# Performance work log

Hardware: AMD Instinct MI355X
Metric: run time of the kernel (lower is better)

The kernel has to match this reference:

```python
import jax, jax.numpy as jnp
import numpy as np

N_EMBED = 40
HEAD_SIZE = 10
N_HEADS = 4
LN_EPS = 1e-5


def _layernorm(x, g, b):
    mu = jnp.mean(x, axis=-1, keepdims=True)
    var = jnp.mean(jnp.square(x - mu), axis=-1, keepdims=True)
    return (x - mu) * jax.lax.rsqrt(var + LN_EPS) * g + b


def setup_inputs() -> dict:
    key = jax.random.key(0)
    ks = jax.random.split(key, 12)
    B, T = 16, 2048
    s = 1.0 / np.sqrt(N_EMBED)
    return {
        "x": jax.random.normal(ks[0], (B, T, N_EMBED), dtype=jnp.float32),
        # per-head Q/K/V weights stacked: [H, n_embed, head_size]
        "Wq": jax.random.normal(ks[1], (N_HEADS, N_EMBED, HEAD_SIZE), dtype=jnp.float32) * s,
        "Wk": jax.random.normal(ks[2], (N_HEADS, N_EMBED, HEAD_SIZE), dtype=jnp.float32) * s,
        "Wv": jax.random.normal(ks[3], (N_HEADS, N_EMBED, HEAD_SIZE), dtype=jnp.float32) * s,
        "Wp": jax.random.normal(ks[4], (N_EMBED, N_EMBED), dtype=jnp.float32) * s,
        "bp": jnp.zeros((N_EMBED,), dtype=jnp.float32),
        "W1": jax.random.normal(ks[5], (N_EMBED, N_EMBED), dtype=jnp.float32) * s,
        "b1": jnp.zeros((N_EMBED,), dtype=jnp.float32),
        "W2": jax.random.normal(ks[6], (N_EMBED, N_EMBED), dtype=jnp.float32) * s,
        "b2": jnp.zeros((N_EMBED,), dtype=jnp.float32),
        "g1": jnp.ones((N_EMBED,), dtype=jnp.float32),
        "be1": jnp.zeros((N_EMBED,), dtype=jnp.float32),
        "g2": jnp.ones((N_EMBED,), dtype=jnp.float32),
        "be2": jnp.zeros((N_EMBED,), dtype=jnp.float32),
    }


def reference(x, Wq, Wk, Wv, Wp, bp, W1, b1, W2, b2, g1, be1, g2, be2):
    B, T, D = x.shape
    # --- pre-norm (note: original overwrites x, so residual uses ln1(x)) ---
    x = _layernorm(x, g1, be1)
    # --- multi-head attention (faithful to source: scores = k @ q^T, no scale, no mask) ---
    q = jnp.einsum("btd,hde->bhte", x, Wq)  # [B,H,T,hs]
    k = jnp.einsum("btd,hde->bhte", x, Wk)
    v = jnp.einsum("btd,hde->bhte", x, Wv)
    w = jnp.einsum("bhie,bhje->bhij", k, q)  # k @ q.transpose(-2,-1)
    w = jax.nn.softmax(w, axis=-1)
    out = jnp.einsum("bhij,bhje->bhie", w, v)  # [B,H,T,hs]
    out = jnp.transpose(out, (0, 2, 1, 3)).reshape(B, T, D)  # concat heads
    out = out @ Wp + bp
    x = x + out
    # --- second norm + FFN (residual uses ln2(x), as in source) ---
    x = _layernorm(x, g2, be2)
    h = jax.nn.relu(x @ W1 + b1)
    x = x + (h @ W2 + b2)
    return x
```

## Files before the change

### kernel.cpp

```cpp
#include <hip/hip_runtime.h>
#include <math.h>

namespace {

using bf16x8 = __attribute__((ext_vector_type(8))) short;
using f32x4  = __attribute__((ext_vector_type(4))) float;

constexpr int D   = 40;
constexpr int HS  = 10;
constexpr int NH  = 4;
constexpr int TT  = 2048;
constexpr int BB  = 16;
constexpr int ROWS = BB * TT;
constexpr int PE  = 16;
constexpr int VR  = 11;
constexpr float LOG2E = 1.4426950408889634f;

__device__ inline unsigned short f2b(float x) {
    unsigned int u = __float_as_uint(x);
    unsigned int r = (u + 0x7fffu + ((u >> 16) & 1u)) >> 16;
    return (unsigned short)r;
}

__device__ inline f32x4 mfma32(bf16x8 a, bf16x8 b, f32x4 c) {
    return __builtin_amdgcn_mfma_f32_16x16x32_bf16(a, b, c, 0, 0, 0);
}

__device__ inline float dot40(const float* __restrict__ xr,
                              const float* __restrict__ w) {
    float s0 = 0.f, s1 = 0.f, s2 = 0.f, s3 = 0.f;
    const float4* w4 = reinterpret_cast<const float4*>(w);
    #pragma unroll
    for (int i = 0; i < 10; ++i) {
        float4 t = w4[i];
        s0 = fmaf(xr[4*i+0], t.x, s0);
        s1 = fmaf(xr[4*i+1], t.y, s1);
        s2 = fmaf(xr[4*i+2], t.z, s2);
        s3 = fmaf(xr[4*i+3], t.w, s3);
    }
    return (s0 + s1) + (s2 + s3);
}

__global__ __launch_bounds__(256) void k_ln_qkv(
    const float* __restrict__ x,  const float* __restrict__ Wq,
    const float* __restrict__ Wk, const float* __restrict__ Wv,
    const float* __restrict__ g1, const float* __restrict__ be1,
    float* __restrict__ xn, unsigned short* __restrict__ qb,
    unsigned short* __restrict__ kb, unsigned short* __restrict__ vT)
{
    __shared__ float wt_s[3*NH*HS*D];
    __shared__ float g_s[D], b_s[D];
    const int tid = threadIdx.x;
    for (int i = tid; i < NH*D*HS; i += 256) {
        const int h = i / (D*HS), r = i % (D*HS);
        const int d = r / HS, e = r % HS;
        const int to = (h*HS + e)*D + d;
        wt_s[to]              = Wq[i];
        wt_s[NH*HS*D + to]    = Wk[i];
        wt_s[2*NH*HS*D + to]  = Wv[i];
    }
    if (tid < D) { g_s[tid] = g1[tid]; b_s[tid] = be1[tid]; }
    __syncthreads();

    const int gid = blockIdx.x * 256 + tid;
    const int row = gid >> 2;
    const int h   = gid & 3;

    float xr[D];
    const float4* xp = reinterpret_cast<const float4*>(x + (size_t)row * D);
    #pragma unroll
    for (int i = 0; i < D/4; ++i) {
        float4 t4 = xp[i];
        xr[4*i+0]=t4.x; xr[4*i+1]=t4.y; xr[4*i+2]=t4.z; xr[4*i+3]=t4.w;
    }
    float mu = 0.f;
    #pragma unroll
    for (int d = 0; d < D; ++d) mu += xr[d];
    mu *= (1.f/D);
    float var = 0.f;
    #pragma unroll
    for (int d = 0; d < D; ++d) { float dd = xr[d]-mu; var += dd*dd; }
    var *= (1.f/D);
    const float rs = rsqrtf(var + 1e-5f);
    #pragma unroll
    for (int d = 0; d < D; ++d) xr[d] = (xr[d]-mu)*rs*g_s[d] + b_s[d];

    if (h == 0) {
        float4* xo = reinterpret_cast<float4*>(xn + (size_t)row * D);
        #pragma unroll
        for (int i = 0; i < D/4; ++i) {
            float4 t4; t4.x=xr[4*i+0]; t4.y=xr[4*i+1]; t4.z=xr[4*i+2]; t4.w=xr[4*i+3];
            xo[i] = t4;
        }
    }

    const int b = row >> 11;
    const int t = row & (TT-1);
    const int bh = b*NH + h;

    float aq[HS], ak[HS], av[HS];
    #pragma unroll
    for (int e = 0; e < HS; ++e) {
        aq[e] = dot40(xr, &wt_s[(h*HS + e)*D]);
        ak[e] = dot40(xr, &wt_s[NH*HS*D + (h*HS + e)*D]);
        av[e] = dot40(xr, &wt_s[2*NH*HS*D + (h*HS + e)*D]);
    }

    union { unsigned short u[PE]; uint4 v4[2]; } Uq, Uk;
    #pragma unroll
    for (int e = 0; e < PE; ++e) {
        Uq.u[e] = (e < HS) ? f2b(aq[e] * LOG2E) : (unsigned short)0;
        Uk.u[e] = (e < HS) ? f2b(ak[e]) : (unsigned short)0;
    }
    uint4* qp4 = reinterpret_cast<uint4*>(qb + ((size_t)bh*TT + t)*PE);
    uint4* kp4 = reinterpret_cast<uint4*>(kb + ((size_t)bh*TT + t)*PE);
    qp4[0] = Uq.v4[0]; qp4[1] = Uq.v4[1];
    kp4[0] = Uk.v4[0]; kp4[1] = Uk.v4[1];
    #pragma unroll
    for (int e = 0; e < HS; ++e)
        vT[((size_t)bh*VR + e)*TT + t] = f2b(av[e]);
    vT[((size_t)bh*VR + HS)*TT + t] = 0x3F80;
}

__global__ __launch_bounds__(256, 4) void k_attn(
    const unsigned short* __restrict__ qb, const unsigned short* __restrict__ kb,
    const unsigned short* __restrict__ vT, float* __restrict__ ao)
{
    __shared__ __align__(16) unsigned short PT[4][2][16][40];
    const int w    = threadIdx.x >> 6;
    const int lane = threadIdx.x & 63;
    const int g    = lane >> 4;
    const int li   = lane & 15;
    const int bh   = blockIdx.y;
    const int i0   = blockIdx.x * 64 + w * 16;
    const size_t bT = (size_t)bh * TT;

    const bf16x8 zero8 = {0,0,0,0,0,0,0,0};
    const f32x4  zacc  = {0.f,0.f,0.f,0.f};

    bf16x8 kf = zero8;
    if (g < 2) kf = *reinterpret_cast<const bf16x8*>(kb + (bT + i0 + li)*PE + 8*g);

    f32x4 accA = zacc, accB = zacc;
    const unsigned short* vrow = vT + ((size_t)bh*VR + (li <= HS ? li : 0))*TT;
    const unsigned short* qrow = qb + (bT + li)*PE + 8*g;

    for (int it = 0; it < TT/64; ++it) {
        const int jA = it * 32;
        const int jB = jA + TT/2;

        bf16x8 a0A=zero8, a1A=zero8, a0B=zero8, a1B=zero8;
        if (g < 2) {
            a0A = *reinterpret_cast<const bf16x8*>(qrow + (size_t)(jA     )*PE);
            a1A = *reinterpret_cast<const bf16x8*>(qrow + (size_t)(jA + 16)*PE);
            a0B = *reinterpret_cast<const bf16x8*>(qrow + (size_t)(jB     )*PE);
            a1B = *reinterpret_cast<const bf16x8*>(qrow + (size_t)(jB + 16)*PE);
        }
        bf16x8 vfA=zero8, vfB=zero8;
        if (li <= HS) {
            vfA = *reinterpret_cast<const bf16x8*>(vrow + jA + 8*g);
            vfB = *reinterpret_cast<const bf16x8*>(vrow + jB + 8*g);
        }

        f32x4 sA0 = mfma32(a0A, kf, zacc);
        f32x4 sA1 = mfma32(a1A, kf, zacc);
        f32x4 sB0 = mfma32(a0B, kf, zacc);
        f32x4 sB1 = mfma32(a1B, kf, zacc);

        const float pA0 = __builtin_amdgcn_exp2f(sA0[0]), pA1 = __builtin_amdgcn_exp2f(sA0[1]);
        const float pA2 = __builtin_amdgcn_exp2f(sA0[2]), pA3 = __builtin_amdgcn_exp2f(sA0[3]);
        const float pA4 = __builtin_amdgcn_exp2f(sA1[0]), pA5 = __builtin_amdgcn_exp2f(sA1[1]);
        const float pA6 = __builtin_amdgcn_exp2f(sA1[2]), pA7 = __builtin_amdgcn_exp2f(sA1[3]);
        const float pB0 = __builtin_amdgcn_exp2f(sB0[0]), pB1 = __builtin_amdgcn_exp2f(sB0[1]);
        const float pB2 = __builtin_amdgcn_exp2f(sB0[2]), pB3 = __builtin_amdgcn_exp2f(sB0[3]);
        const float pB4 = __builtin_amdgcn_exp2f(sB1[0]), pB5 = __builtin_amdgcn_exp2f(sB1[1]);
        const float pB6 = __builtin_amdgcn_exp2f(sB1[2]), pB7 = __builtin_amdgcn_exp2f(sB1[3]);

        unsigned int wA0,wA1,wA2,wA3, wB0,wB1,wB2,wB3;
        asm("v_cvt_pk_bf16_f32 %0, %1, %2" : "=v"(wA0) : "v"(pA0), "v"(pA1));
        asm("v_cvt_pk_bf16_f32 %0, %1, %2" : "=v"(wA1) : "v"(pA2), "v"(pA3));
        asm("v_cvt_pk_bf16_f32 %0, %1, %2" : "=v"(wA2) : "v"(pA4), "v"(pA5));
        asm("v_cvt_pk_bf16_f32 %0, %1, %2" : "=v"(wA3) : "v"(pA6), "v"(pA7));
        asm("v_cvt_pk_bf16_f32 %0, %1, %2" : "=v"(wB0) : "v"(pB0), "v"(pB1));
        asm("v_cvt_pk_bf16_f32 %0, %1, %2" : "=v"(wB1) : "v"(pB2), "v"(pB3));
        asm("v_cvt_pk_bf16_f32 %0, %1, %2" : "=v"(wB2) : "v"(pB4), "v"(pB5));
        asm("v_cvt_pk_bf16_f32 %0, %1, %2" : "=v"(wB3) : "v"(pB6), "v"(pB7));

        *reinterpret_cast<uint2*>(&PT[w][0][li][4*g])      = make_uint2(wA0, wA1);
        *reinterpret_cast<uint2*>(&PT[w][0][li][16 + 4*g]) = make_uint2(wA2, wA3);
        *reinterpret_cast<uint2*>(&PT[w][1][li][4*g])      = make_uint2(wB0, wB1);
        *reinterpret_cast<uint2*>(&PT[w][1][li][16 + 4*g]) = make_uint2(wB2, wB3);

        bf16x8 pfA = *reinterpret_cast<const bf16x8*>(&PT[w][0][li][8*g]);
        bf16x8 pfB = *reinterpret_cast<const bf16x8*>(&PT[w][1][li][8*g]);

        accA = mfma32(vfA, pfA, accA);
        accB = mfma32(vfB, pfB, accB);
    }

    const f32x4 acc = accA + accB;
    const float l = __shfl(acc[2], 32 + li);
    const float linv = 1.f / l;
    float* orow = ao + (bT + i0 + li) * HS;
    #pragma unroll
    for (int r = 0; r < 4; ++r) {
        const int e = 4*g + r;
        if (e < HS) orow[e] = acc[r] * linv;
    }
}

__global__ __launch_bounds__(256) void k_epilogue(
    const float* __restrict__ attn, const float* __restrict__ xn,
    const float* __restrict__ Wp, const float* __restrict__ bp,
    const float* __restrict__ W1, const float* __restrict__ b1,
    const float* __restrict__ W2, const float* __restrict__ b2,
    const float* __restrict__ g2, const float* __restrict__ be2,
    float* __restrict__ out)
{
    __shared__ float wp_s[D*D], w1_s[D*D], w2_s[D*D];
    __shared__ float bp_s[D], b1_s[D], b2_s[D], g_s[D], be_s[D];
    const int tid = threadIdx.x;
    for (int i = tid; i < D*D; i += 256) { wp_s[i]=Wp[i]; w1_s[i]=W1[i]; w2_s[i]=W2[i]; }
    if (tid < D) {
        bp_s[tid]=bp[tid]; b1_s[tid]=b1[tid]; b2_s[tid]=b2[tid];
        g_s[tid]=g2[tid]; be_s[tid]=be2[tid];
    }
    __syncthreads();

    const int gid  = blockIdx.x * 256 + tid;
    const int row  = gid >> 1;
    const int half = gid & 1;
    const int b0   = half * 20;
    const int b    = row >> 11;
    const int t    = row & (TT-1);

    float cat[D];
    #pragma unroll
    for (int h = 0; h < NH; ++h) {
        const float2* ap = reinterpret_cast<const float2*>(
            attn + ((((size_t)b*NH + h)*TT) + t)*HS);
        #pragma unroll
        for (int e = 0; e < HS/2; ++e) {
            float2 t2 = ap[e];
            cat[h*HS + 2*e] = t2.x; cat[h*HS + 2*e + 1] = t2.y;
        }
    }

    float y[20];
    {
        const float4* xp = reinterpret_cast<const float4*>(xn + (size_t)row*D + b0);
        #pragma unroll
        for (int i = 0; i < 5; ++i) {
            float4 t4 = xp[i];
            y[4*i+0]=t4.x; y[4*i+1]=t4.y; y[4*i+2]=t4.z; y[4*i+3]=t4.w;
        }
    }
    #pragma unroll
    for (int d = 0; d < 20; ++d) y[d] += bp_s[b0+d];
    for (int c = 0; c < D; ++c) {
        const float cc = cat[c];
        const float4* wr = reinterpret_cast<const float4*>(&wp_s[c*D + b0]);
        #pragma unroll
        for (int i = 0; i < 5; ++i) {
            float4 t4 = wr[i];
            y[4*i+0] = fmaf(cc, t4.x, y[4*i+0]);
            y[4*i+1] = fmaf(cc, t4.y, y[4*i+1]);
            y[4*i+2] = fmaf(cc, t4.z, y[4*i+2]);
            y[4*i+3] = fmaf(cc, t4.w, y[4*i+3]);
        }
    }

    float sp = 0.f;
    #pragma unroll
    for (int d = 0; d < 20; ++d) sp += y[d];
    const float mu = (sp + __shfl_xor(sp, 1)) * (1.f/D);
    float vp = 0.f;
    #pragma unroll
    for (int d = 0; d < 20; ++d) { float dd = y[d]-mu; vp += dd*dd; }
    const float var = (vp + __shfl_xor(vp, 1)) * (1.f/D);
    const float rs = rsqrtf(var + 1e-5f);

    float y2[20];
    #pragma unroll
    for (int d = 0; d < 20; ++d) y2[d] = (y[d]-mu)*rs*g_s[b0+d] + be_s[b0+d];

    float z[D];
    {
        const int ob0 = 20 - b0;
        #pragma unroll
        for (int d = 0; d < 20; ++d) {
            z[b0 + d]  = y2[d];
            z[ob0 + d] = __shfl_xor(y2[d], 1);
        }
    }

    float hd[20];
    #pragma unroll
    for (int d = 0; d < 20; ++d) hd[d] = b1_s[b0+d];
    for (int c = 0; c < D; ++c) {
        const float cc = z[c];
        const float4* wr = reinterpret_cast<const float4*>(&w1_s[c*D + b0]);
        #pragma unroll
        for (int i = 0; i < 5; ++i) {
            float4 t4 = wr[i];
            hd[4*i+0] = fmaf(cc, t4.x, hd[4*i+0]);
            hd[4*i+1] = fmaf(cc, t4.y, hd[4*i+1]);
            hd[4*i+2] = fmaf(cc, t4.z, hd[4*i+2]);
            hd[4*i+3] = fmaf(cc, t4.w, hd[4*i+3]);
        }
    }
    #pragma unroll
    for (int d = 0; d < 20; ++d) hd[d] = fmaxf(hd[d], 0.f);

    float hf[D];
    {
        const int ob0 = 20 - b0;
        #pragma unroll
        for (int d = 0; d < 20; ++d) {
            hf[b0 + d]  = hd[d];
            hf[ob0 + d] = __shfl_xor(hd[d], 1);
        }
    }

    float ov[20];
    #pragma unroll
    for (int d = 0; d < 20; ++d) ov[d] = y2[d] + b2_s[b0+d];
    for (int c = 0; c < D; ++c) {
        const float cc = hf[c];
        const float4* wr = reinterpret_cast<const float4*>(&w2_s[c*D + b0]);
        #pragma unroll
        for (int i = 0; i < 5; ++i) {
            float4 t4 = wr[i];
            ov[4*i+0] = fmaf(cc, t4.x, ov[4*i+0]);
            ov[4*i+1] = fmaf(cc, t4.y, ov[4*i+1]);
            ov[4*i+2] = fmaf(cc, t4.z, ov[4*i+2]);
            ov[4*i+3] = fmaf(cc, t4.w, ov[4*i+3]);
        }
    }

    float4* op = reinterpret_cast<float4*>(out + (size_t)row*D + b0);
    #pragma unroll
    for (int i = 0; i < 5; ++i) {
        float4 t4; t4.x=ov[4*i+0]; t4.y=ov[4*i+1]; t4.z=ov[4*i+2]; t4.w=ov[4*i+3];
        op[i] = t4;
    }
}

}

extern "C" void kernel_launch(void* const* d_in, const int* in_sizes, int n_in,
                              void* d_out, int out_size, void* d_ws, size_t ws_size,
                              hipStream_t stream) {
    const float* x   = (const float*)d_in[0];
    const float* Wq  = (const float*)d_in[1];
    const float* Wk  = (const float*)d_in[2];
    const float* Wv  = (const float*)d_in[3];
    const float* Wp  = (const float*)d_in[4];
    const float* bp  = (const float*)d_in[5];
    const float* W1  = (const float*)d_in[6];
    const float* b1  = (const float*)d_in[7];
    const float* W2  = (const float*)d_in[8];
    const float* b2  = (const float*)d_in[9];
    const float* g1  = (const float*)d_in[10];
    const float* be1 = (const float*)d_in[11];
    const float* g2  = (const float*)d_in[12];
    const float* be2 = (const float*)d_in[13];

    const size_t N = (size_t)ROWS * D;
    float* xn = (float*)d_ws;
    float* ao = xn + N;
    unsigned short* qb = (unsigned short*)(ao + N);
    unsigned short* kb = qb + (size_t)BB*NH*TT*PE;
    unsigned short* vT = kb + (size_t)BB*NH*TT*PE;

    k_ln_qkv<<<ROWS*4/256, 256, 0, stream>>>(x, Wq, Wk, Wv, g1, be1, xn, qb, kb, vT);
    k_attn<<<dim3(TT/64, BB*NH), 256, 0, stream>>>(qb, kb, vT, ao);
    k_epilogue<<<ROWS*2/256, 256, 0, stream>>>(ao, xn, Wp, bp, W1, b1, W2, b2, g2, be2,
                                               (float*)d_out);
}
```

Before: 119.7 us.

## Split QKV and epilogue work across more threads, software-pipeline attention loads

The QKV kernel now assigns eight threads per row, two per head, each computing five of the ten head dims and swapping Q/K halves via a lane shuffle so each thread writes one packed row. The epilogue splits each row across four threads instead of two, using cross-lane shuffles to rebuild the full vectors. The attention loop prefetches the next iteration's Q/V fragments into registers, wraps the MFMAs in s_setprio, and drops the occupancy hint from launch_bounds. These changes aim for more parallelism and latency hiding, at the cost of redundant LayerNorm work and extra shuffles.

```diff
diff --git a/kernel.cpp b/kernel.cpp
--- a/kernel.cpp
+++ b/kernel.cpp
@@ -63,8 +63,9 @@
     __syncthreads();
 
     const int gid = blockIdx.x * 256 + tid;
-    const int row = gid >> 2;
-    const int h   = gid & 3;
+    const int eh  = gid & 1;
+    const int h   = (gid >> 1) & 3;
+    const int row = gid >> 3;
 
     float xr[D];
     const float4* xp = reinterpret_cast<const float4*>(x + (size_t)row * D);
@@ -85,7 +86,7 @@
     #pragma unroll
     for (int d = 0; d < D; ++d) xr[d] = (xr[d]-mu)*rs*g_s[d] + b_s[d];
 
-    if (h == 0) {
+    if ((gid & 7) == 0) {
         float4* xo = reinterpret_cast<float4*>(xn + (size_t)row * D);
         #pragma unroll
         for (int i = 0; i < D/4; ++i) {
@@ -97,32 +98,45 @@
     const int b = row >> 11;
     const int t = row & (TT-1);
     const int bh = b*NH + h;
-
-    float aq[HS], ak[HS], av[HS];
-    #pragma unroll
-    for (int e = 0; e < HS; ++e) {
-        aq[e] = dot40(xr, &wt_s[(h*HS + e)*D]);
-        ak[e] = dot40(xr, &wt_s[NH*HS*D + (h*HS + e)*D]);
-        av[e] = dot40(xr, &wt_s[2*NH*HS*D + (h*HS + e)*D]);
-    }
-
-    union { unsigned short u[PE]; uint4 v4[2]; } Uq, Uk;
-    #pragma unroll
-    for (int e = 0; e < PE; ++e) {
-        Uq.u[e] = (e < HS) ? f2b(aq[e] * LOG2E) : (unsigned short)0;
-        Uk.u[e] = (e < HS) ? f2b(ak[e]) : (unsigned short)0;
-    }
-    uint4* qp4 = reinterpret_cast<uint4*>(qb + ((size_t)bh*TT + t)*PE);
-    uint4* kp4 = reinterpret_cast<uint4*>(kb + ((size_t)bh*TT + t)*PE);
-    qp4[0] = Uq.v4[0]; qp4[1] = Uq.v4[1];
-    kp4[0] = Uk.v4[0]; kp4[1] = Uk.v4[1];
-    #pragma unroll
-    for (int e = 0; e < HS; ++e)
-        vT[((size_t)bh*VR + e)*TT + t] = f2b(av[e]);
-    vT[((size_t)bh*VR + HS)*TT + t] = 0x3F80;
-}
-
-__global__ __launch_bounds__(256, 4) void k_attn(
+    const int e0 = eh * 5;
+
+    float aq[5], ak[5], av[5];
+    #pragma unroll
+    for (int e = 0; e < 5; ++e) {
+        aq[e] = dot40(xr, &wt_s[(h*HS + e0 + e)*D]);
+        ak[e] = dot40(xr, &wt_s[NH*HS*D + (h*HS + e0 + e)*D]);
+        av[e] = dot40(xr, &wt_s[2*NH*HS*D + (h*HS + e0 + e)*D]);
+    }
+
+    float send[5], recv[5];
+    #pragma unroll
+    for (int j = 0; j < 5; ++j) send[j] = eh ? aq[j] : ak[j];
+    #pragma unroll
+    for (int j = 0; j < 5; ++j) recv[j] = __shfl_xor(send[j], 1);
+
+    const float scale = eh ? 1.f : LOG2E;
+    float lo[5], hi[5];
+    #pragma unroll
+    for (int j = 0; j < 5; ++j) {
+        lo[j] = eh ? recv[j] : aq[j];
+        hi[j] = eh ? ak[j]   : recv[j];
+    }
+    union { unsigned short u[PE]; uint4 v4[2]; } U;
+    #pragma unroll
+    for (int e = 0; e < PE; ++e)
+        U.u[e] = (e < 5) ? f2b(lo[e]*scale)
+               : (e < 10) ? f2b(hi[e-5]*scale) : (unsigned short)0;
+    unsigned short* dst = (eh ? kb : qb) + ((size_t)bh*TT + t)*PE;
+    uint4* d4 = reinterpret_cast<uint4*>(dst);
+    d4[0] = U.v4[0]; d4[1] = U.v4[1];
+
+    #pragma unroll
+    for (int e = 0; e < 5; ++e)
+        vT[((size_t)bh*VR + e0 + e)*TT + t] = f2b(av[e]);
+    if (eh) vT[((size_t)bh*VR + HS)*TT + t] = 0x3F80;
+}
+
+__global__ __launch_bounds__(256) void k_attn(
     const unsigned short* __restrict__ qb, const unsigned short* __restrict__ kb,
     const unsigned short* __restrict__ vT, float* __restrict__ ao)
 {
@@ -142,30 +156,45 @@
     if (g < 2) kf = *reinterpret_cast<const bf16x8*>(kb + (bT + i0 + li)*PE + 8*g);
 
     f32x4 accA = zacc, accB = zacc;
+    const bool qok = (g < 2), vok = (li <= HS);
     const unsigned short* vrow = vT + ((size_t)bh*VR + (li <= HS ? li : 0))*TT;
     const unsigned short* qrow = qb + (bT + li)*PE + 8*g;
 
+    bf16x8 a0A=zero8, a1A=zero8, a0B=zero8, a1B=zero8, vfA=zero8, vfB=zero8;
+    if (qok) {
+        a0A = *reinterpret_cast<const bf16x8*>(qrow);
+        a1A = *reinterpret_cast<const bf16x8*>(qrow + (size_t)16*PE);
+        a0B = *reinterpret_cast<const bf16x8*>(qrow + (size_t)(TT/2)*PE);
+        a1B = *reinterpret_cast<const bf16x8*>(qrow + (size_t)(TT/2 + 16)*PE);
+    }
+    if (vok) {
+        vfA = *reinterpret_cast<const bf16x8*>(vrow + 8*g);
+        vfB = *reinterpret_cast<const bf16x8*>(vrow + TT/2 + 8*g);
+    }
+
     for (int it = 0; it < TT/64; ++it) {
-        const int jA = it * 32;
-        const int jB = jA + TT/2;
-
-        bf16x8 a0A=zero8, a1A=zero8, a0B=zero8, a1B=zero8;
-        if (g < 2) {
-            a0A = *reinterpret_cast<const bf16x8*>(qrow + (size_t)(jA     )*PE);
-            a1A = *reinterpret_cast<const bf16x8*>(qrow + (size_t)(jA + 16)*PE);
-            a0B = *reinterpret_cast<const bf16x8*>(qrow + (size_t)(jB     )*PE);
-            a1B = *reinterpret_cast<const bf16x8*>(qrow + (size_t)(jB + 16)*PE);
-        }
-        bf16x8 vfA=zero8, vfB=zero8;
-        if (li <= HS) {
-            vfA = *reinterpret_cast<const bf16x8*>(vrow + jA + 8*g);
-            vfB = *reinterpret_cast<const bf16x8*>(vrow + jB + 8*g);
-        }
-
+        const int nit = (it + 1) & (TT/64 - 1);
+        const int njA = nit * 32;
+        const int njB = njA + TT/2;
+
+        __builtin_amdgcn_s_setprio(1);
         f32x4 sA0 = mfma32(a0A, kf, zacc);
         f32x4 sA1 = mfma32(a1A, kf, zacc);
         f32x4 sB0 = mfma32(a0B, kf, zacc);
         f32x4 sB1 = mfma32(a1B, kf, zacc);
+        __builtin_amdgcn_s_setprio(0);
+
+        bf16x8 n0A=zero8, n1A=zero8, n0B=zero8, n1B=zero8, nvA=zero8, nvB=zero8;
+        if (qok) {
+            n0A = *reinterpret_cast<const bf16x8*>(qrow + (size_t)(njA     )*PE);
+            n1A = *reinterpret_cast<const bf16x8*>(qrow + (size_t)(njA + 16)*PE);
+            n0B = *reinterpret_cast<const bf16x8*>(qrow + (size_t)(njB     )*PE);
+            n1B = *reinterpret_cast<const bf16x8*>(qrow + (size_t)(njB + 16)*PE);
+        }
+        if (vok) {
+            nvA = *reinterpret_cast<const bf16x8*>(vrow + njA + 8*g);
+            nvB = *reinterpret_cast<const bf16x8*>(vrow + njB + 8*g);
+        }
 
         const float pA0 = __builtin_amdgcn_exp2f(sA0[0]), pA1 = __builtin_amdgcn_exp2f(sA0[1]);
         const float pA2 = __builtin_amdgcn_exp2f(sA0[2]), pA3 = __builtin_amdgcn_exp2f(sA0[3]);
@@ -194,8 +223,12 @@
         bf16x8 pfA = *reinterpret_cast<const bf16x8*>(&PT[w][0][li][8*g]);
         bf16x8 pfB = *reinterpret_cast<const bf16x8*>(&PT[w][1][li][8*g]);
 
+        __builtin_amdgcn_s_setprio(1);
         accA = mfma32(vfA, pfA, accA);
         accB = mfma32(vfB, pfB, accB);
+        __builtin_amdgcn_s_setprio(0);
+
+        a0A = n0A; a1A = n1A; a0B = n0B; a1B = n1B; vfA = nvA; vfB = nvB;
     }
 
     const f32x4 acc = accA + accB;
@@ -228,9 +261,11 @@
     __syncthreads();
 
     const int gid  = blockIdx.x * 256 + tid;
-    const int row  = gid >> 1;
-    const int half = gid & 1;
-    const int b0   = half * 20;
+    const int row  = gid >> 2;
+    const int q4   = gid & 3;
+    const int b0   = q4 * 10;
+    const int lane = tid & 63;
+    const int base = lane & 60;
     const int b    = row >> 11;
     const int t    = row & (TT-1);
 
@@ -246,103 +281,80 @@
         }
     }
 
-    float y[20];
+    float y[10];
     {
-        const float4* xp = reinterpret_cast<const float4*>(xn + (size_t)row*D + b0);
+        const float2* xp = reinterpret_cast<const float2*>(xn + (size_t)row*D + b0);
         #pragma unroll
         for (int i = 0; i < 5; ++i) {
-            float4 t4 = xp[i];
-            y[4*i+0]=t4.x; y[4*i+1]=t4.y; y[4*i+2]=t4.z; y[4*i+3]=t4.w;
-        }
-    }
-    #pragma unroll
-    for (int d = 0; d < 20; ++d) y[d] += bp_s[b0+d];
+            float2 t2 = xp[i];
+            y[2*i+0] = t2.x; y[2*i+1] = t2.y;
+        }
+    }
+    #pragma unroll
+    for (int d = 0; d < 10; ++d) y[d] += bp_s[b0+d];
     for (int c = 0; c < D; ++c) {
         const float cc = cat[c];
-        const float4* wr = reinterpret_cast<const float4*>(&wp_s[c*D + b0]);
-        #pragma unroll
-        for (int i = 0; i < 5; ++i) {
-            float4 t4 = wr[i];
-            y[4*i+0] = fmaf(cc, t4.x, y[4*i+0]);
-            y[4*i+1] = fmaf(cc, t4.y, y[4*i+1]);
-            y[4*i+2] = fmaf(cc, t4.z, y[4*i+2]);
-            y[4*i+3] = fmaf(cc, t4.w, y[4*i+3]);
-        }
+        const float* wr = &wp_s[c*D + b0];
+        #pragma unroll
+        for (int d = 0; d < 10; ++d) y[d] = fmaf(cc, wr[d], y[d]);
     }
 
     float sp = 0.f;
     #pragma unroll
-    for (int d = 0; d < 20; ++d) sp += y[d];
-    const float mu = (sp + __shfl_xor(sp, 1)) * (1.f/D);
+    for (int d = 0; d < 10; ++d) sp += y[d];
+    sp += __shfl_xor(sp, 1); sp += __shfl_xor(sp, 2);
+    const float mu = sp * (1.f/D);
     float vp = 0.f;
     #pragma unroll
-    for (int d = 0; d < 20; ++d) { float dd = y[d]-mu; vp += dd*dd; }
-    const float var = (vp + __shfl_xor(vp, 1)) * (1.f/D);
-    const float rs = rsqrtf(var + 1e-5f);
-
-    float y2[20];
-    #pragma unroll
-    for (int d = 0; d < 20; ++d) y2[d] = (y[d]-mu)*rs*g_s[b0+d] + be_s[b0+d];
+    for (int d = 0; d < 10; ++d) { float dd = y[d]-mu; vp += dd*dd; }
+    vp += __shfl_xor(vp, 1); vp += __shfl_xor(vp, 2);
+    const float rs = rsqrtf(vp * (1.f/D) + 1e-5f);
+
+    float y2[10];
+    #pragma unroll
+    for (int d = 0; d < 10; ++d) y2[d] = (y[d]-mu)*rs*g_s[b0+d] + be_s[b0+d];
 
     float z[D];
-    {
-        const int ob0 = 20 - b0;
-        #pragma unroll
-        for (int d = 0; d < 20; ++d) {
-            z[b0 + d]  = y2[d];
-            z[ob0 + d] = __shfl_xor(y2[d], 1);
-        }
-    }
-
-    float hd[20];
-    #pragma unroll
-    for (int d = 0; d < 20; ++d) hd[d] = b1_s[b0+d];
+    #pragma unroll
+    for (int seg = 0; seg < 4; ++seg)
+        #pragma unroll
+        for (int j = 0; j < 10; ++j)
+            z[seg*10 + j] = __shfl(y2[j], base + seg);
+
+    float hd[10];
+    #pragma unroll
+    for (int d = 0; d < 10; ++d) hd[d] = b1_s[b0+d];
     for (int c = 0; c < D; ++c) {
         const float cc = z[c];
-        const float4* wr = reinterpret_cast<const float4*>(&w1_s[c*D + b0]);
-        #pragma unroll
-        for (int i = 0; i < 5; ++i) {
-            float4 t4 = wr[i];
-            hd[4*i+0] = fmaf(cc, t4.x, hd[4*i+0]);
-            hd[4*i+1] = fmaf(cc, t4.y, hd[4*i+1]);
-            hd[4*i+2] = fmaf(cc, t4.z, hd[4*i+2]);
-            hd[4*i+3] = fmaf(cc, t4.w, hd[4*i+3]);
-        }
-    }
-    #pragma unroll
-    for (int d = 0; d < 20; ++d) hd[d] = fmaxf(hd[d], 0.f);
+        const float* wr = &w1_s[c*D + b0];
+        #pragma unroll
+        for (int d = 0; d < 10; ++d) hd[d] = fmaf(cc, wr[d], hd[d]);
+    }
+    #pragma unroll
+    for (int d = 0; d < 10; ++d) hd[d] = fmaxf(hd[d], 0.f);
 
     float hf[D];
-    {
-        const int ob0 = 20 - b0;
-        #pragma unroll
-        for (int d = 0; d < 20; ++d) {
-            hf[b0 + d]  = hd[d];
-            hf[ob0 + d] = __shfl_xor(hd[d], 1);
-        }
-    }
-
-    float ov[20];
-    #pragma unroll
-    for (int d = 0; d < 20; ++d) ov[d] = y2[d] + b2_s[b0+d];
+    #pragma unroll
+    for (int seg = 0; seg < 4; ++seg)
+        #pragma unroll
+        for (int j = 0; j < 10; ++j)
+            hf[seg*10 + j] = __shfl(hd[j], base + seg);
+
+    float ov[10];
+    #pragma unroll
+    for (int d = 0; d < 10; ++d) ov[d] = y2[d] + b2_s[b0+d];
     for (int c = 0; c < D; ++c) {
         const float cc = hf[c];
-        const float4* wr = reinterpret_cast<const float4*>(&w2_s[c*D + b0]);
-        #pragma unroll
-        for (int i = 0; i < 5; ++i) {
-            float4 t4 = wr[i];
-            ov[4*i+0] = fmaf(cc, t4.x, ov[4*i+0]);
-            ov[4*i+1] = fmaf(cc, t4.y, ov[4*i+1]);
-            ov[4*i+2] = fmaf(cc, t4.z, ov[4*i+2]);
-            ov[4*i+3] = fmaf(cc, t4.w, ov[4*i+3]);
-        }
-    }
-
-    float4* op = reinterpret_cast<float4*>(out + (size_t)row*D + b0);
+        const float* wr = &w2_s[c*D + b0];
+        #pragma unroll
+        for (int d = 0; d < 10; ++d) ov[d] = fmaf(cc, wr[d], ov[d]);
+    }
+
+    float2* op = reinterpret_cast<float2*>(out + (size_t)row*D + b0);
     #pragma unroll
     for (int i = 0; i < 5; ++i) {
-        float4 t4; t4.x=ov[4*i+0]; t4.y=ov[4*i+1]; t4.z=ov[4*i+2]; t4.w=ov[4*i+3];
-        op[i] = t4;
+        float2 t2; t2.x = ov[2*i]; t2.y = ov[2*i+1];
+        op[i] = t2;
     }
 }
 
@@ -373,8 +385,8 @@
     unsigned short* kb = qb + (size_t)BB*NH*TT*PE;
     unsigned short* vT = kb + (size_t)BB*NH*TT*PE;
 
-    k_ln_qkv<<<ROWS*4/256, 256, 0, stream>>>(x, Wq, Wk, Wv, g1, be1, xn, qb, kb, vT);
+    k_ln_qkv<<<ROWS*8/256, 256, 0, stream>>>(x, Wq, Wk, Wv, g1, be1, xn, qb, kb, vT);
     k_attn<<<dim3(TT/64, BB*NH), 256, 0, stream>>>(qb, kb, vT, ao);
-    k_epilogue<<<ROWS*2/256, 256, 0, stream>>>(ao, xn, Wp, bp, W1, b1, W2, b2, g2, be2,
+    k_epilogue<<<ROWS*4/256, 256, 0, stream>>>(ao, xn, Wp, bp, W1, b1, W2, b2, g2, be2,
                                                (float*)d_out);
 }
```

New measurement: 117.2 us. 2.1% less time.
